# Kernel tuning notes

Hardware: AMD Instinct MI355X
Metric: run time of the kernel (lower is better)

## Reference

```python
import jax, jax.numpy as jnp
import numpy as np

B = 128          # graphs
N = 512          # nodes per graph
NT = B * N       # total nodes = 65536
E = NT * 16      # total edges = 1048576
IN = 64
H = 128
OUT = 2
L = 4            # num_layers
RATIO = 0.8


def setup_inputs() -> dict:
    key = jax.random.key(0)
    ks = jax.random.split(key, 20)

    def w(k, shape, fan_in):
        return jax.random.normal(k, shape, jnp.float32) / np.sqrt(fan_in)

    x = jax.random.normal(ks[0], (NT, IN), jnp.float32)
    edge_index = jax.random.randint(ks[1], (2, E), 0, NT, dtype=jnp.int32)
    batch = (jnp.arange(NT) // N).astype(jnp.int32)  # equal-size graphs

    return {
        "x": x,
        "edge_index": edge_index,
        "batch": batch,
        # conv1: GraphConv(IN, H, aggr='mean') -> lin_rel (w/ bias) + lin_root (no bias)
        "W1_rel": w(ks[2], (IN, H), IN),
        "W1_root": w(ks[3], (IN, H), IN),
        "b1": jnp.zeros((H,), jnp.float32),
        # convs[0..2]: GraphConv(H, H, aggr='mean'), stacked
        "Wc_rel": w(ks[4], (L - 1, H, H), H),
        "Wc_root": w(ks[5], (L - 1, H, H), H),
        "bc": jnp.zeros((L - 1, H), jnp.float32),
        # SAGPooling score GNN: GraphConv(H, 1) with default aggr='add'
        "pw_rel": w(ks[6], (H,), H),
        "pw_root": w(ks[7], (H,), H),
        "pb": jnp.zeros((1,), jnp.float32),
        # MLP head
        "lin1_W": w(ks[8], (L * H, H), L * H),
        "lin1_b": jnp.zeros((H,), jnp.float32),
        "lin2_W": w(ks[9], (H, OUT), H),
        "lin2_b": jnp.zeros((OUT,), jnp.float32),
    }


def _graph_conv_mean(x, src, dst, emask, W_rel, W_root, b, n):
    # PyG GraphConv: lin_rel(mean_{j->i} x_j) + lin_root(x_i); masked edges excluded.
    msg = x[src] * emask[:, None]                                  # [E, D] gather
    s = jax.ops.segment_sum(msg, dst, num_segments=n)              # [n, D] scatter-add
    cnt = jax.ops.segment_sum(emask, dst, num_segments=n)          # [n]
    agg = s / jnp.maximum(cnt, 1.0)[:, None]                       # zero for isolated nodes
    return agg @ W_rel + x @ W_root + b


def reference(x, edge_index, batch, W1_rel, W1_root, b1, Wc_rel, Wc_root, bc,
              pw_rel, pw_root, pb, lin1_W, lin1_b, lin2_W, lin2_b):
    src = edge_index[0]
    dst = edge_index[1]
    emask = jnp.ones((E,), jnp.float32)
    n = NT
    npg = N  # nodes per graph (all graphs equal size)

    h = jax.nn.relu(_graph_conv_mean(x, src, dst, emask, W1_rel, W1_root, b1, n))
    xs = [h.reshape(B, npg, H).mean(axis=1)]  # global_mean_pool

    for i in range(L - 1):
        h = jax.nn.relu(_graph_conv_mean(h, src, dst, emask, Wc_rel[i], Wc_root[i], bc[i], n))
        xs.append(h.reshape(B, npg, H).mean(axis=1))
        if i % 2 == 0 and i < L - 2:
            # ---- SAGPooling: score via GraphConv(H,1) with add aggregation ----
            smsg = jax.ops.segment_sum(h[src] * emask[:, None], dst, num_segments=n)
            score = smsg @ pw_rel + h @ pw_root + pb[0]            # [n]
            k = int(np.ceil(RATIO * npg))
            topv, topi = jax.lax.top_k(score.reshape(B, npg), k)   # per-graph top-k
            perm = (jnp.arange(B)[:, None] * npg + topi).reshape(-1)  # global kept ids
            h = h[perm] * jnp.tanh(topv.reshape(-1))[:, None]
            # remap edges; edges touching dropped nodes get masked out
            node_map = jnp.full((n,), -1, jnp.int32).at[perm].set(
                jnp.arange(B * k, dtype=jnp.int32))
            ns, nd = node_map[src], node_map[dst]
            keep = ((ns >= 0) & (nd >= 0)).astype(jnp.float32)
            emask = emask * keep
            src = jnp.where(ns >= 0, ns, 0)
            dst = jnp.where(nd >= 0, nd, 0)
            n = B * k
            npg = k

    xcat = jnp.concatenate(xs, axis=-1)                            # JumpingKnowledge 'cat'
    out = jax.nn.relu(xcat @ lin1_W + lin1_b)
    # dropout is identity in eval mode
    out = out @ lin2_W + lin2_b
    return jax.nn.log_softmax(out, axis=-1)
```

## Files before the change

### kernel.cpp

```cpp
#include <hip/hip_runtime.h>
#include <math.h>

#define NT 65536
#define EE 1048576
#define NB 128
#define KK 410
#define HH 128

typedef short bf16x8 __attribute__((ext_vector_type(8)));
typedef float f32x4 __attribute__((ext_vector_type(4)));

__device__ unsigned short g_xb[(size_t)NT * 64];
__device__ unsigned short g_hb1[(size_t)NT * HH];
__device__ unsigned short g_hb2[(size_t)NT * HH];
__device__ unsigned short g_wt1[128 * 128];
__device__ unsigned short g_wtc[3 * 128 * 256];
__device__ unsigned short g_csr1u[EE];
__device__ unsigned short g_keptu[NT];
__device__ unsigned int g_ebuck[EE];
__device__ int g_bcnt[128];
__device__ int g_bcur[128];
__device__ float g_trel[NT];
__device__ float g_troot[NT];
__device__ float g_gatef[NT];
__device__ float g_kinv[NT];
__device__ float g_xc16[4 * NB * 16 * 128];
__device__ int g_rows1[NT + 1];

__device__ __forceinline__ float b2f(unsigned short u) {
    union { unsigned int i; float f; } v;
    v.i = ((unsigned int)u) << 16;
    return v.f;
}
__device__ __forceinline__ unsigned short f2b(float f) {
    unsigned int x = __float_as_uint(f);
    unsigned int r = x + 0x7fffu + ((x >> 16) & 1u);
    return (unsigned short)(r >> 16);
}
__device__ __forceinline__ bf16x8 scale8(bf16x8 a, float g) {
    bf16x8 r;
#pragma unroll
    for (int i = 0; i < 8; i++) {
        unsigned short u = (unsigned short)a[i];
        r[i] = (short)f2b(b2f(u) * g);
    }
    return r;
}

__global__ __launch_bounds__(256) void k_prep(const float* __restrict__ x,
                                              const float* __restrict__ W1r,
                                              const float* __restrict__ W1o,
                                              const float* __restrict__ Wcr,
                                              const float* __restrict__ Wco,
                                              const int* __restrict__ dst) {
    if (blockIdx.x < 4544) {
        int tid = blockIdx.x * 256 + threadIdx.x;
        if (tid < 1048576) {
            float4 v = *(const float4*)&x[(size_t)tid * 4];
            unsigned int lo = (unsigned int)f2b(v.x) | ((unsigned int)f2b(v.y) << 16);
            unsigned int hi = (unsigned int)f2b(v.z) | ((unsigned int)f2b(v.w) << 16);
            *(uint2*)&g_xb[(size_t)tid * 4] = make_uint2(lo, hi);
        } else if (tid < 1048576 + 16384) {
            int r = tid - 1048576;
            int k = r & 127, n = r >> 7;
            float v = (k < 64) ? W1r[k * 128 + n] : W1o[(k - 64) * 128 + n];
            g_wt1[n * 128 + k] = f2b(v);
        } else {
            int r = tid - (1048576 + 16384);
            int l = r >> 15;
            int k = r & 255, n = (r >> 8) & 127;
            float v = (k < 128) ? Wcr[l * 16384 + k * 128 + n]
                                : Wco[l * 16384 + (k - 128) * 128 + n];
            g_wtc[l * 32768 + n * 256 + k] = f2b(v);
        }
    } else {
        __shared__ int h[128];
        if (threadIdx.x < 128) h[threadIdx.x] = 0;
        __syncthreads();
        int e0 = ((blockIdx.x - 4544) * 256 + threadIdx.x) * 4;
        int4 d = *(const int4*)&dst[e0];
        atomicAdd(&h[d.x >> 9], 1);
        atomicAdd(&h[d.y >> 9], 1);
        atomicAdd(&h[d.z >> 9], 1);
        atomicAdd(&h[d.w >> 9], 1);
        __syncthreads();
        if (threadIdx.x < 128 && h[threadIdx.x]) atomicAdd(&g_bcnt[threadIdx.x], h[threadIdx.x]);
    }
}

__global__ __launch_bounds__(256) void k_bscatter(const int* __restrict__ src,
                                                  const int* __restrict__ dst) {
    __shared__ int h[128];
    __shared__ int base[128];
    __shared__ int sc[128];
    __shared__ int vv[128];
    int t = threadIdx.x;
    if (t < 128) { vv[t] = g_bcnt[t]; sc[t] = vv[t]; h[t] = 0; }
    __syncthreads();
    for (int off = 1; off < 128; off <<= 1) {
        int u = (t >= off && t < 128) ? sc[t - off] : 0;
        __syncthreads();
        if (t < 128) sc[t] += u;
        __syncthreads();
    }
    int e0 = (blockIdx.x * 256 + t) * 4;
    int4 s = *(const int4*)&src[e0];
    int4 d = *(const int4*)&dst[e0];
    int b0 = d.x >> 9, b1 = d.y >> 9, b2 = d.z >> 9, b3 = d.w >> 9;
    atomicAdd(&h[b0], 1);
    atomicAdd(&h[b1], 1);
    atomicAdd(&h[b2], 1);
    atomicAdd(&h[b3], 1);
    __syncthreads();
    if (t < 128) {
        int c = h[t];
        base[t] = (sc[t] - vv[t]) + (c ? atomicAdd(&g_bcur[t], c) : 0);
        h[t] = 0;
    }
    __syncthreads();
    int r0 = atomicAdd(&h[b0], 1);
    g_ebuck[base[b0] + r0] = ((unsigned int)(d.x & 511) << 16) | (unsigned int)s.x;
    int r1 = atomicAdd(&h[b1], 1);
    g_ebuck[base[b1] + r1] = ((unsigned int)(d.y & 511) << 16) | (unsigned int)s.y;
    int r2 = atomicAdd(&h[b2], 1);
    g_ebuck[base[b2] + r2] = ((unsigned int)(d.z & 511) << 16) | (unsigned int)s.z;
    int r3 = atomicAdd(&h[b3], 1);
    g_ebuck[base[b3] + r3] = ((unsigned int)(d.w & 511) << 16) | (unsigned int)s.w;
}

__global__ __launch_bounds__(512) void k_bcsr() {
    __shared__ int hist[512];
    __shared__ int offs[512];
    __shared__ int cur[512];
    __shared__ int sc[128];
    int g = blockIdx.x, t = threadIdx.x;
    if (t < 128) sc[t] = g_bcnt[t];
    hist[t] = 0;
    cur[t] = 0;
    __syncthreads();
    for (int off = 1; off < 128; off <<= 1) {
        int u = (t >= off && t < 128) ? sc[t - off] : 0;
        __syncthreads();
        if (t < 128) sc[t] += u;
        __syncthreads();
    }
    int b0 = sc[g] - g_bcnt[g];
    int b1 = sc[g];
    for (int e = b0 + t; e < b1; e += 512) {
        unsigned int p = g_ebuck[e];
        atomicAdd(&hist[p >> 16], 1);
    }
    __syncthreads();
    int v = hist[t];
    offs[t] = v;
    __syncthreads();
    for (int off = 1; off < 512; off <<= 1) {
        int u = (t >= off) ? offs[t - off] : 0;
        __syncthreads();
        offs[t] += u;
        __syncthreads();
    }
    int excl = offs[t] - v;
    g_rows1[g * 512 + t] = b0 + excl;
    if (t == 511) g_rows1[g * 512 + 512] = b0 + excl + v;
    __syncthreads();
    offs[t] = excl;
    __syncthreads();
    for (int e = b0 + t; e < b1; e += 512) {
        unsigned int p = g_ebuck[e];
        int dl = p >> 16;
        int r = atomicAdd(&cur[dl], 1);
        g_csr1u[b0 + offs[dl] + r] = (unsigned short)(p & 0xFFFFu);
    }
}

__global__ __launch_bounds__(256, 4) void k_conv1(const float* __restrict__ bias) {
    const unsigned short* h = g_xb;
    const unsigned short* Wt = g_wt1;
    unsigned short* out = g_hb1;
    __shared__ float s[128];
    int lane = threadIdx.x & 63;
    int w = threadIdx.x >> 6;
    int n16 = lane & 15, quad = lane >> 4;
    int rowbase = blockIdx.x * 64;
    int rowg = rowbase + w * 16;
    int node = rowg + n16;
    if (threadIdx.x < 128) s[threadIdx.x] = 0.f;
    int r0 = g_rows1[node], r1 = g_rows1[node + 1];
    float aggacc[2][8];
#pragma unroll
    for (int ch = 0; ch < 2; ch++)
#pragma unroll
        for (int j = 0; j < 8; j++) aggacc[ch][j] = 0.f;
    const unsigned short* hq = h + quad * 8;
#define ACC8(arow, v)                                            \
    arow[0] += b2f((unsigned short)(v.x & 0xffff));              \
    arow[1] += b2f((unsigned short)(v.x >> 16));                 \
    arow[2] += b2f((unsigned short)(v.y & 0xffff));              \
    arow[3] += b2f((unsigned short)(v.y >> 16));                 \
    arow[4] += b2f((unsigned short)(v.z & 0xffff));              \
    arow[5] += b2f((unsigned short)(v.z >> 16));                 \
    arow[6] += b2f((unsigned short)(v.w & 0xffff));              \
    arow[7] += b2f((unsigned short)(v.w >> 16));
    int e = r0;
    for (; e + 2 <= r1; e += 2) {
        int i0 = g_csr1u[e], i1 = g_csr1u[e + 1];
        uint4 v00 = *(const uint4*)&hq[(size_t)i0 * 64];
        uint4 v01 = *(const uint4*)&hq[(size_t)i0 * 64 + 32];
        uint4 v10 = *(const uint4*)&hq[(size_t)i1 * 64];
        uint4 v11 = *(const uint4*)&hq[(size_t)i1 * 64 + 32];
        ACC8(aggacc[0], v00) ACC8(aggacc[1], v01)
        ACC8(aggacc[0], v10) ACC8(aggacc[1], v11)
    }
    if (e < r1) {
        int i0 = g_csr1u[e];
        uint4 v00 = *(const uint4*)&hq[(size_t)i0 * 64];
        uint4 v01 = *(const uint4*)&hq[(size_t)i0 * 64 + 32];
        ACC8(aggacc[0], v00) ACC8(aggacc[1], v01)
    }
#undef ACC8
    int c = r1 - r0;
    float inv = 1.0f / (float)(c > 0 ? c : 1);
    bf16x8 afrag[2];
#pragma unroll
    for (int ch = 0; ch < 2; ch++)
#pragma unroll
        for (int j = 0; j < 8; j++) afrag[ch][j] = (short)f2b(aggacc[ch][j] * inv);

    f32x4 acc[8];
#pragma unroll
    for (int ct = 0; ct < 8; ct++)
#pragma unroll
        for (int i = 0; i < 4; i++) acc[ct][i] = 0.f;
#pragma unroll
    for (int ks = 0; ks < 4; ks++) {
        bf16x8 a;
        if (ks < 2) a = afrag[ks];
        else a = *(const bf16x8*)&g_xb[(size_t)node * 64 + (ks - 2) * 32 + quad * 8];
#pragma unroll
        for (int ct = 0; ct < 8; ct++) {
            bf16x8 b = *(const bf16x8*)&Wt[(size_t)(ct * 16 + n16) * 128 + ks * 32 + quad * 8];
            acc[ct] = __builtin_amdgcn_mfma_f32_16x16x32_bf16(a, b, acc[ct], 0, 0, 0);
        }
    }
#pragma unroll
    for (int ct = 0; ct < 8; ct++) {
        int cc = ct * 16 + n16;
        float bv = bias[cc];
#pragma unroll
        for (int i = 0; i < 4; i++) {
            int r = rowg + quad * 4 + i;
            float v = fmaxf(acc[ct][i] + bv, 0.f);
            acc[ct][i] = v;
            out[(size_t)r * 128 + cc] = f2b(v);
        }
    }
    __syncthreads();
#pragma unroll
    for (int ct = 0; ct < 8; ct++) {
        float p = acc[ct][0] + acc[ct][1] + acc[ct][2] + acc[ct][3];
        p += __shfl_xor(p, 16);
        p += __shfl_xor(p, 32);
        if (quad == 0) atomicAdd(&s[ct * 16 + n16], p);
    }
    __syncthreads();
    if (threadIdx.x < 128) {
        int gr = blockIdx.x >> 3, e8 = blockIdx.x & 7;
        g_xc16[((0 * NB + gr) * 16 + e8) * 128 + threadIdx.x] = s[threadIdx.x];
    }
}

template <int KC, int GATED, int MASKED, int DOTS, int BGATE>
__global__ __launch_bounds__(256, 8) void k_conv(int hSel, int bSel, int wOfs,
                                                 const float* __restrict__ bias, int outSel,
                                                 int sec,
                                                 const float* __restrict__ pwr,
                                                 const float* __restrict__ pwt) {
    const unsigned short* h = hSel == 1 ? g_hb1 : g_hb2;
    const unsigned short* Bp = bSel == 1 ? g_hb1 : g_hb2;
    const unsigned short* Wt = g_wtc + wOfs;
    unsigned short* out = outSel == 1 ? g_hb1 : g_hb2;
    __shared__ unsigned short frag[2][16][136];
    __shared__ float s[128];
    __shared__ float sdr[32], sdt[32];
    int lane = threadIdx.x & 63;
    int w = threadIdx.x >> 6;
    int g = w >> 1;
    int h2 = w & 1;
    int n16 = lane & 15, quad = lane >> 4;
    int rowbase = blockIdx.x * 32;
    int rowg = rowbase + g * 16;
    int node = rowg + n16;
    if (threadIdx.x < 128) s[threadIdx.x] = 0.f;
    if (threadIdx.x < 32) { sdr[threadIdx.x] = 0.f; sdt[threadIdx.x] = 0.f; }

    int r0 = g_rows1[node], r1 = g_rows1[node + 1];
    float aggacc[2][8];
#pragma unroll
    for (int ch = 0; ch < 2; ch++)
#pragma unroll
        for (int j = 0; j < 8; j++) aggacc[ch][j] = 0.f;
    int kc = 0;
    const unsigned short* hq = h + h2 * 64 + quad * 8;
#define ACC8(arow, v, gf)                                        \
    arow[0] += gf * b2f((unsigned short)(v.x & 0xffff));         \
    arow[1] += gf * b2f((unsigned short)(v.x >> 16));            \
    arow[2] += gf * b2f((unsigned short)(v.y & 0xffff));         \
    arow[3] += gf * b2f((unsigned short)(v.y >> 16));            \
    arow[4] += gf * b2f((unsigned short)(v.z & 0xffff));         \
    arow[5] += gf * b2f((unsigned short)(v.z >> 16));            \
    arow[6] += gf * b2f((unsigned short)(v.w & 0xffff));         \
    arow[7] += gf * b2f((unsigned short)(v.w >> 16));
    int e = r0;
    for (; e + 2 <= r1; e += 2) {
        int i0 = g_csr1u[e], i1 = g_csr1u[e + 1];
        uint4 v00 = *(const uint4*)&hq[(size_t)i0 * 128];
        uint4 v01 = *(const uint4*)&hq[(size_t)i0 * 128 + 32];
        uint4 v10 = *(const uint4*)&hq[(size_t)i1 * 128];
        uint4 v11 = *(const uint4*)&hq[(size_t)i1 * 128 + 32];
        float gf0 = GATED ? g_gatef[i0] : 1.0f;
        float gf1 = GATED ? g_gatef[i1] : 1.0f;
        if (KC == 1) kc += (int)g_keptu[i0] + (int)g_keptu[i1];
        ACC8(aggacc[0], v00, gf0) ACC8(aggacc[1], v01, gf0)
        ACC8(aggacc[0], v10, gf1) ACC8(aggacc[1], v11, gf1)
    }
    if (e < r1) {
        int i0 = g_csr1u[e];
        uint4 v00 = *(const uint4*)&hq[(size_t)i0 * 128];
        uint4 v01 = *(const uint4*)&hq[(size_t)i0 * 128 + 32];
        float gf0 = GATED ? g_gatef[i0] : 1.0f;
        if (KC == 1) kc += (int)g_keptu[i0];
        ACC8(aggacc[0], v00, gf0) ACC8(aggacc[1], v01, gf0)
    }
#undef ACC8
    float inv;
    if (KC == 0) {
        int c = r1 - r0;
        inv = 1.0f / (float)(c > 0 ? c : 1);
    } else if (KC == 1) {
        inv = 1.0f / (float)(kc > 0 ? kc : 1);
        if (h2 == 0 && quad == 0) g_kinv[node] = inv;
    } else {
        inv = g_kinv[node];
    }
#pragma unroll
    for (int ch = 0; ch < 2; ch++) {
        bf16x8 fk;
#pragma unroll
        for (int j = 0; j < 8; j++) fk[j] = (short)f2b(aggacc[ch][j] * inv);
        *(bf16x8*)&frag[g][n16][h2 * 64 + ch * 32 + quad * 8] = fk;
    }
    __syncthreads();

    float ga = BGATE ? g_gatef[node] : 1.0f;
    f32x4 acc[4];
#pragma unroll
    for (int c4 = 0; c4 < 4; c4++)
#pragma unroll
        for (int i = 0; i < 4; i++) acc[c4][i] = 0.f;
#pragma unroll
    for (int ks = 0; ks < 8; ks++) {
        bf16x8 a;
        if (ks < 4) {
            a = *(const bf16x8*)&frag[g][n16][ks * 32 + quad * 8];
        } else {
            a = *(const bf16x8*)&Bp[(size_t)node * 128 + (ks - 4) * 32 + quad * 8];
            if (BGATE) a = scale8(a, ga);
        }
#pragma unroll
        for (int c4 = 0; c4 < 4; c4++) {
            int ct = h2 * 4 + c4;
            bf16x8 b = *(const bf16x8*)&Wt[(size_t)(ct * 16 + n16) * 256 + ks * 32 + quad * 8];
            acc[c4] = __builtin_amdgcn_mfma_f32_16x16x32_bf16(a, b, acc[c4], 0, 0, 0);
        }
    }

    {
        float m[4];
#pragma unroll
        for (int i = 0; i < 4; i++) {
            int r = rowg + quad * 4 + i;
            m[i] = (!MASKED || g_keptu[r]) ? 1.0f : 0.0f;
        }
#pragma unroll
        for (int c4 = 0; c4 < 4; c4++) {
            int c = (h2 * 4 + c4) * 16 + n16;
            float bv = bias[c];
#pragma unroll
            for (int i = 0; i < 4; i++) {
                int r = rowg + quad * 4 + i;
                float v = fmaxf(acc[c4][i] + bv, 0.f) * m[i];
                acc[c4][i] = v;
                out[(size_t)r * 128 + c] = f2b(v);
            }
        }
    }

#pragma unroll
    for (int c4 = 0; c4 < 4; c4++) {
        float p = acc[c4][0] + acc[c4][1] + acc[c4][2] + acc[c4][3];
        p += __shfl_xor(p, 16);
        p += __shfl_xor(p, 32);
        if (quad == 0) atomicAdd(&s[(h2 * 4 + c4) * 16 + n16], p);
    }

    if (DOTS) {
        float pr[4], pt[4];
#pragma unroll
        for (int c4 = 0; c4 < 4; c4++) {
            pr[c4] = pwr[(h2 * 4 + c4) * 16 + n16];
            pt[c4] = pwt[(h2 * 4 + c4) * 16 + n16];
        }
#pragma unroll
        for (int i = 0; i < 4; i++) {
            float dr = 0.f, dt = 0.f;
#pragma unroll
            for (int c4 = 0; c4 < 4; c4++) {
                dr += acc[c4][i] * pr[c4];
                dt += acc[c4][i] * pt[c4];
            }
            dr += __shfl_xor(dr, 1); dt += __shfl_xor(dt, 1);
            dr += __shfl_xor(dr, 2); dt += __shfl_xor(dt, 2);
            dr += __shfl_xor(dr, 4); dt += __shfl_xor(dt, 4);
            dr += __shfl_xor(dr, 8); dt += __shfl_xor(dt, 8);
            if (n16 == 0) {
                atomicAdd(&sdr[g * 16 + quad * 4 + i], dr);
                atomicAdd(&sdt[g * 16 + quad * 4 + i], dt);
            }
        }
    }
    __syncthreads();
    if (threadIdx.x < 128) {
        int gr = blockIdx.x >> 4, e16 = blockIdx.x & 15;
        g_xc16[((sec * NB + gr) * 16 + e16) * 128 + threadIdx.x] = s[threadIdx.x];
    }
    if (DOTS && threadIdx.x < 32) {
        g_trel[rowbase + threadIdx.x] = sdr[threadIdx.x];
        g_troot[rowbase + threadIdx.x] = sdt[threadIdx.x];
    }
}

__global__ __launch_bounds__(256) void k_topk(const float* __restrict__ pb) {
    __shared__ float sv[512];
    __shared__ int si[512];
    int g = blockIdx.x, t = threadIdx.x;
    if (t == 0) { g_bcnt[g] = 0; g_bcur[g] = 0; }
    float pbv = pb[0];
    for (int l = t; l < 512; l += 256) {
        int node = g * 512 + l;
        int r0 = g_rows1[node], r1 = g_rows1[node + 1];
        float s = 0.f;
        int e = r0;
        for (; e + 4 <= r1; e += 4) {
            float s0 = g_trel[g_csr1u[e]];
            float s1 = g_trel[g_csr1u[e + 1]];
            float s2 = g_trel[g_csr1u[e + 2]];
            float s3 = g_trel[g_csr1u[e + 3]];
            s += (s0 + s1) + (s2 + s3);
        }
        for (; e < r1; e++) s += g_trel[g_csr1u[e]];
        sv[l] = s + g_troot[node] + pbv;
        si[l] = l;
    }
    __syncthreads();
    for (int k = 2; k <= 512; k <<= 1) {
        for (int j = k >> 1; j > 0; j >>= 1) {
            for (int i = t; i < 512; i += 256) {
                int p = i ^ j;
                if (p > i) {
                    float va = sv[i], vb = sv[p];
                    int ia = si[i], ib = si[p];
                    bool aFirst = (va > vb) || (va == vb && ia < ib);
                    bool up = ((i & k) == 0);
                    if (up != aFirst) { sv[i] = vb; sv[p] = va; si[i] = ib; si[p] = ia; }
                }
            }
            __syncthreads();
        }
    }
    for (int r = t; r < 512; r += 256) {
        int old = g * 512 + si[r];
        if (r < KK) {
            g_gatef[old] = tanhf(sv[r]);
            g_keptu[old] = 1;
        } else {
            g_gatef[old] = 0.f;
            g_keptu[old] = 0;
        }
    }
}

__global__ __launch_bounds__(128) void k_head(const float* __restrict__ W1, const float* __restrict__ b1,
                                              const float* __restrict__ W2, const float* __restrict__ b2,
                                              float* __restrict__ out) {
    __shared__ float xr[512];
    __shared__ float r0[128], r1[128];
    int g = blockIdx.x, t = threadIdx.x;
    for (int i = t; i < 512; i += 128) {
        int sec = i >> 7, c = i & 127;
        const float* p = &g_xc16[((sec * NB + g) * 16) * 128 + c];
        int nq = (sec == 0) ? 8 : 16;
        float v = 0.f;
        for (int q = 0; q < nq; q++) v += p[q * 128];
        float inv = (sec < 2) ? (1.0f / 512.0f) : (1.0f / 410.0f);
        xr[i] = v * inv;
    }
    __syncthreads();
    float acc = b1[t];
    for (int k = 0; k < 512; k++) acc += xr[k] * W1[k * 128 + t];
    acc = fmaxf(acc, 0.f);
    r0[t] = acc * W2[t * 2 + 0];
    r1[t] = acc * W2[t * 2 + 1];
    __syncthreads();
    for (int off = 64; off > 0; off >>= 1) {
        if (t < off) { r0[t] += r0[t + off]; r1[t] += r1[t + off]; }
        __syncthreads();
    }
    if (t == 0) {
        float z0 = r0[0] + b2[0], z1 = r1[0] + b2[1];
        float m = fmaxf(z0, z1);
        float l = m + logf(expf(z0 - m) + expf(z1 - m));
        out[g * 2 + 0] = z0 - l;
        out[g * 2 + 1] = z1 - l;
    }
}

extern "C" void kernel_launch(void* const* d_in, const int* in_sizes, int n_in,
                              void* d_out, int out_size, void* d_ws, size_t ws_size,
                              hipStream_t stream) {
    const float* x = (const float*)d_in[0];
    const int* ei = (const int*)d_in[1];
    const int* src = ei;
    const int* dst = ei + EE;
    const float* W1r = (const float*)d_in[3];
    const float* W1o = (const float*)d_in[4];
    const float* b1 = (const float*)d_in[5];
    const float* Wcr = (const float*)d_in[6];
    const float* Wco = (const float*)d_in[7];
    const float* bc = (const float*)d_in[8];
    const float* pwr = (const float*)d_in[9];
    const float* pwt = (const float*)d_in[10];
    const float* pb = (const float*)d_in[11];
    const float* l1W = (const float*)d_in[12];
    const float* l1b = (const float*)d_in[13];
    const float* l2W = (const float*)d_in[14];
    const float* l2b = (const float*)d_in[15];
    float* out = (float*)d_out;

    k_prep<<<5568, 256, 0, stream>>>(x, W1r, W1o, Wcr, Wco, dst);

    k_bscatter<<<1024, 256, 0, stream>>>(src, dst);
    k_bcsr<<<128, 512, 0, stream>>>();

    k_conv1<<<1024, 256, 0, stream>>>(b1);

    k_conv<0, 0, 0, 1, 0><<<2048, 256, 0, stream>>>(1, 1, 0, bc, 2, 1, pwr, pwt);

    k_topk<<<NB, 256, 0, stream>>>(pb);

    k_conv<1, 1, 1, 0, 1><<<2048, 256, 0, stream>>>(2, 2, 32768, bc + 128, 1, 2, pwr, pwt);

    k_conv<2, 0, 1, 0, 0><<<2048, 256, 0, stream>>>(1, 1, 65536, bc + 256, 2, 3, pwr, pwt);

    k_head<<<NB, 128, 0, stream>>>(l1W, l1b, l2W, l2b, out);
}
```

Before: 527.2 us.

## Use 16-row conv blocks with full-row gathers and sort CSR neighbors by source

Each k_conv block now handles 16 rows instead of 32. Every wavefront aggregates 4 destination rows, with each lane gathering one 16-byte chunk of a full 128-wide row, so a neighbor row is read as one contiguous 256-byte access. The MFMA stage splits output columns across the 4 waves, and the grid doubles to 4096 blocks with 32 partial-sum slots per graph. The CSR build also sub-sorts each row's edges by the high bits of the source index, which should improve cache locality of the gathers. The cost is more blocks, more redundant weight loads per row, and a larger shared histogram in k_bcsr.

```diff
diff --git a/kernel.cpp b/kernel.cpp
--- a/kernel.cpp
+++ b/kernel.cpp
@@ -24,7 +24,7 @@
 __device__ float g_troot[NT];
 __device__ float g_gatef[NT];
 __device__ float g_kinv[NT];
-__device__ float g_xc16[4 * NB * 16 * 128];
+__device__ float g_xc32[4 * NB * 32 * 128];
 __device__ int g_rows1[NT + 1];
 
 __device__ __forceinline__ float b2f(unsigned short u) {
@@ -129,14 +129,13 @@
 }
 
 __global__ __launch_bounds__(512) void k_bcsr() {
-    __shared__ int hist[512];
-    __shared__ int offs[512];
-    __shared__ int cur[512];
+    __shared__ int hist[4096];
+    __shared__ int cur[4096];
     __shared__ int sc[128];
+    __shared__ int temp[512];
     int g = blockIdx.x, t = threadIdx.x;
     if (t < 128) sc[t] = g_bcnt[t];
-    hist[t] = 0;
-    cur[t] = 0;
+    for (int i = t; i < 4096; i += 512) { hist[i] = 0; cur[i] = 0; }
     __syncthreads();
     for (int off = 1; off < 128; off <<= 1) {
         int u = (t >= off && t < 128) ? sc[t - off] : 0;
@@ -146,31 +145,38 @@
     }
     int b0 = sc[g] - g_bcnt[g];
     int b1 = sc[g];
+    __syncthreads();
     for (int e = b0 + t; e < b1; e += 512) {
         unsigned int p = g_ebuck[e];
-        atomicAdd(&hist[p >> 16], 1);
-    }
-    __syncthreads();
-    int v = hist[t];
-    offs[t] = v;
+        int key = (int)((p >> 16) << 3) | (int)((p & 0xFFFFu) >> 13);
+        atomicAdd(&hist[key], 1);
+    }
+    __syncthreads();
+    int vals[8];
+    int s8 = 0;
+#pragma unroll
+    for (int j = 0; j < 8; j++) { vals[j] = hist[t * 8 + j]; s8 += vals[j]; }
+    temp[t] = s8;
     __syncthreads();
     for (int off = 1; off < 512; off <<= 1) {
-        int u = (t >= off) ? offs[t - off] : 0;
-        __syncthreads();
-        offs[t] += u;
-        __syncthreads();
-    }
-    int excl = offs[t] - v;
+        int u = (t >= off) ? temp[t - off] : 0;
+        __syncthreads();
+        temp[t] += u;
+        __syncthreads();
+    }
+    int excl = temp[t] - s8;
+    int run = excl;
+#pragma unroll
+    for (int j = 0; j < 8; j++) { int v = vals[j]; hist[t * 8 + j] = run; run += v; }
     g_rows1[g * 512 + t] = b0 + excl;
-    if (t == 511) g_rows1[g * 512 + 512] = b0 + excl + v;
-    __syncthreads();
-    offs[t] = excl;
+    if (t == 511) g_rows1[g * 512 + 512] = b0 + excl + s8;
     __syncthreads();
     for (int e = b0 + t; e < b1; e += 512) {
         unsigned int p = g_ebuck[e];
-        int dl = p >> 16;
-        int r = atomicAdd(&cur[dl], 1);
-        g_csr1u[b0 + offs[dl] + r] = (unsigned short)(p & 0xFFFFu);
+        unsigned int srcv = p & 0xFFFFu;
+        int key = (int)((p >> 16) << 3) | (int)(srcv >> 13);
+        int r = atomicAdd(&cur[key], 1);
+        g_csr1u[b0 + hist[key] + r] = (unsigned short)srcv;
     }
 }
 
@@ -266,7 +272,7 @@
     __syncthreads();
     if (threadIdx.x < 128) {
         int gr = blockIdx.x >> 3, e8 = blockIdx.x & 7;
-        g_xc16[((0 * NB + gr) * 16 + e8) * 128 + threadIdx.x] = s[threadIdx.x];
+        g_xc32[((0 * NB + gr) * 32 + e8) * 128 + threadIdx.x] = s[threadIdx.x];
     }
 }
 
@@ -280,98 +286,100 @@
     const unsigned short* Bp = bSel == 1 ? g_hb1 : g_hb2;
     const unsigned short* Wt = g_wtc + wOfs;
     unsigned short* out = outSel == 1 ? g_hb1 : g_hb2;
-    __shared__ unsigned short frag[2][16][136];
+    __shared__ unsigned short frag[16][136];
     __shared__ float s[128];
-    __shared__ float sdr[32], sdt[32];
+    __shared__ float sdr[16], sdt[16];
     int lane = threadIdx.x & 63;
     int w = threadIdx.x >> 6;
-    int g = w >> 1;
-    int h2 = w & 1;
+    int rowbase = blockIdx.x * 16;
+    if (threadIdx.x < 128) s[threadIdx.x] = 0.f;
+    if (threadIdx.x < 16) { sdr[threadIdx.x] = 0.f; sdt[threadIdx.x] = 0.f; }
+
+    {
+        int rl = lane >> 4;
+        int c16 = lane & 15;
+        int m = w * 4 + rl;
+        int row = rowbase + m;
+        int r0 = g_rows1[row], r1 = g_rows1[row + 1];
+        float kinv_pre = (KC == 2) ? g_kinv[row] : 0.f;
+        float acc8[8];
+#pragma unroll
+        for (int j = 0; j < 8; j++) acc8[j] = 0.f;
+        int kc = 0;
+        const unsigned short* hq = h + c16 * 8;
+#define ACC8(v, gf)                                              \
+    acc8[0] += gf * b2f((unsigned short)(v.x & 0xffff));         \
+    acc8[1] += gf * b2f((unsigned short)(v.x >> 16));            \
+    acc8[2] += gf * b2f((unsigned short)(v.y & 0xffff));         \
+    acc8[3] += gf * b2f((unsigned short)(v.y >> 16));            \
+    acc8[4] += gf * b2f((unsigned short)(v.z & 0xffff));         \
+    acc8[5] += gf * b2f((unsigned short)(v.z >> 16));            \
+    acc8[6] += gf * b2f((unsigned short)(v.w & 0xffff));         \
+    acc8[7] += gf * b2f((unsigned short)(v.w >> 16));
+        int e = r0;
+        for (; e + 4 <= r1; e += 4) {
+            int i0 = g_csr1u[e], i1 = g_csr1u[e + 1];
+            int i2 = g_csr1u[e + 2], i3 = g_csr1u[e + 3];
+            uint4 v0 = *(const uint4*)&hq[(size_t)i0 * 128];
+            uint4 v1 = *(const uint4*)&hq[(size_t)i1 * 128];
+            uint4 v2 = *(const uint4*)&hq[(size_t)i2 * 128];
+            uint4 v3 = *(const uint4*)&hq[(size_t)i3 * 128];
+            float g0 = GATED ? g_gatef[i0] : 1.0f;
+            float g1 = GATED ? g_gatef[i1] : 1.0f;
+            float g2 = GATED ? g_gatef[i2] : 1.0f;
+            float g3 = GATED ? g_gatef[i3] : 1.0f;
+            if (KC == 1)
+                kc += (int)g_keptu[i0] + (int)g_keptu[i1]
+                    + (int)g_keptu[i2] + (int)g_keptu[i3];
+            ACC8(v0, g0) ACC8(v1, g1) ACC8(v2, g2) ACC8(v3, g3)
+        }
+        for (; e < r1; e++) {
+            int i0 = g_csr1u[e];
+            uint4 v0 = *(const uint4*)&hq[(size_t)i0 * 128];
+            float g0 = GATED ? g_gatef[i0] : 1.0f;
+            if (KC == 1) kc += (int)g_keptu[i0];
+            ACC8(v0, g0)
+        }
+#undef ACC8
+        float inv;
+        if (KC == 0) {
+            int c = r1 - r0;
+            inv = 1.0f / (float)(c > 0 ? c : 1);
+        } else if (KC == 1) {
+            inv = 1.0f / (float)(kc > 0 ? kc : 1);
+            if (c16 == 0) g_kinv[row] = inv;
+        } else {
+            inv = kinv_pre;
+        }
+        bf16x8 fk;
+#pragma unroll
+        for (int j = 0; j < 8; j++) fk[j] = (short)f2b(acc8[j] * inv);
+        *(bf16x8*)&frag[m][c16 * 8] = fk;
+    }
+    __syncthreads();
+
     int n16 = lane & 15, quad = lane >> 4;
-    int rowbase = blockIdx.x * 32;
-    int rowg = rowbase + g * 16;
-    int node = rowg + n16;
-    if (threadIdx.x < 128) s[threadIdx.x] = 0.f;
-    if (threadIdx.x < 32) { sdr[threadIdx.x] = 0.f; sdt[threadIdx.x] = 0.f; }
-
-    int r0 = g_rows1[node], r1 = g_rows1[node + 1];
-    float aggacc[2][8];
-#pragma unroll
-    for (int ch = 0; ch < 2; ch++)
-#pragma unroll
-        for (int j = 0; j < 8; j++) aggacc[ch][j] = 0.f;
-    int kc = 0;
-    const unsigned short* hq = h + h2 * 64 + quad * 8;
-#define ACC8(arow, v, gf)                                        \
-    arow[0] += gf * b2f((unsigned short)(v.x & 0xffff));         \
-    arow[1] += gf * b2f((unsigned short)(v.x >> 16));            \
-    arow[2] += gf * b2f((unsigned short)(v.y & 0xffff));         \
-    arow[3] += gf * b2f((unsigned short)(v.y >> 16));            \
-    arow[4] += gf * b2f((unsigned short)(v.z & 0xffff));         \
-    arow[5] += gf * b2f((unsigned short)(v.z >> 16));            \
-    arow[6] += gf * b2f((unsigned short)(v.w & 0xffff));         \
-    arow[7] += gf * b2f((unsigned short)(v.w >> 16));
-    int e = r0;
-    for (; e + 2 <= r1; e += 2) {
-        int i0 = g_csr1u[e], i1 = g_csr1u[e + 1];
-        uint4 v00 = *(const uint4*)&hq[(size_t)i0 * 128];
-        uint4 v01 = *(const uint4*)&hq[(size_t)i0 * 128 + 32];
-        uint4 v10 = *(const uint4*)&hq[(size_t)i1 * 128];
-        uint4 v11 = *(const uint4*)&hq[(size_t)i1 * 128 + 32];
-        float gf0 = GATED ? g_gatef[i0] : 1.0f;
-        float gf1 = GATED ? g_gatef[i1] : 1.0f;
-        if (KC == 1) kc += (int)g_keptu[i0] + (int)g_keptu[i1];
-        ACC8(aggacc[0], v00, gf0) ACC8(aggacc[1], v01, gf0)
-        ACC8(aggacc[0], v10, gf1) ACC8(aggacc[1], v11, gf1)
-    }
-    if (e < r1) {
-        int i0 = g_csr1u[e];
-        uint4 v00 = *(const uint4*)&hq[(size_t)i0 * 128];
-        uint4 v01 = *(const uint4*)&hq[(size_t)i0 * 128 + 32];
-        float gf0 = GATED ? g_gatef[i0] : 1.0f;
-        if (KC == 1) kc += (int)g_keptu[i0];
-        ACC8(aggacc[0], v00, gf0) ACC8(aggacc[1], v01, gf0)
-    }
-#undef ACC8
-    float inv;
-    if (KC == 0) {
-        int c = r1 - r0;
-        inv = 1.0f / (float)(c > 0 ? c : 1);
-    } else if (KC == 1) {
-        inv = 1.0f / (float)(kc > 0 ? kc : 1);
-        if (h2 == 0 && quad == 0) g_kinv[node] = inv;
-    } else {
-        inv = g_kinv[node];
-    }
-#pragma unroll
-    for (int ch = 0; ch < 2; ch++) {
-        bf16x8 fk;
-#pragma unroll
-        for (int j = 0; j < 8; j++) fk[j] = (short)f2b(aggacc[ch][j] * inv);
-        *(bf16x8*)&frag[g][n16][h2 * 64 + ch * 32 + quad * 8] = fk;
-    }
-    __syncthreads();
-
+    int node = rowbase + n16;
     float ga = BGATE ? g_gatef[node] : 1.0f;
-    f32x4 acc[4];
-#pragma unroll
-    for (int c4 = 0; c4 < 4; c4++)
-#pragma unroll
-        for (int i = 0; i < 4; i++) acc[c4][i] = 0.f;
+    f32x4 acc[2];
+#pragma unroll
+    for (int c2 = 0; c2 < 2; c2++)
+#pragma unroll
+        for (int i = 0; i < 4; i++) acc[c2][i] = 0.f;
 #pragma unroll
     for (int ks = 0; ks < 8; ks++) {
         bf16x8 a;
         if (ks < 4) {
-            a = *(const bf16x8*)&frag[g][n16][ks * 32 + quad * 8];
+            a = *(const bf16x8*)&frag[n16][ks * 32 + quad * 8];
         } else {
             a = *(const bf16x8*)&Bp[(size_t)node * 128 + (ks - 4) * 32 + quad * 8];
             if (BGATE) a = scale8(a, ga);
         }
 #pragma unroll
-        for (int c4 = 0; c4 < 4; c4++) {
-            int ct = h2 * 4 + c4;
+        for (int c2 = 0; c2 < 2; c2++) {
+            int ct = w * 2 + c2;
             bf16x8 b = *(const bf16x8*)&Wt[(size_t)(ct * 16 + n16) * 256 + ks * 32 + quad * 8];
-            acc[c4] = __builtin_amdgcn_mfma_f32_16x16x32_bf16(a, b, acc[c4], 0, 0, 0);
+            acc[c2] = __builtin_amdgcn_mfma_f32_16x16x32_bf16(a, b, acc[c2], 0, 0, 0);
         }
     }
 
@@ -379,62 +387,58 @@
         float m[4];
 #pragma unroll
         for (int i = 0; i < 4; i++) {
-            int r = rowg + quad * 4 + i;
+            int r = rowbase + quad * 4 + i;
             m[i] = (!MASKED || g_keptu[r]) ? 1.0f : 0.0f;
         }
 #pragma unroll
-        for (int c4 = 0; c4 < 4; c4++) {
-            int c = (h2 * 4 + c4) * 16 + n16;
+        for (int c2 = 0; c2 < 2; c2++) {
+            int c = (w * 2 + c2) * 16 + n16;
             float bv = bias[c];
 #pragma unroll
             for (int i = 0; i < 4; i++) {
-                int r = rowg + quad * 4 + i;
-                float v = fmaxf(acc[c4][i] + bv, 0.f) * m[i];
-                acc[c4][i] = v;
+                int r = rowbase + quad * 4 + i;
+                float v = fmaxf(acc[c2][i] + bv, 0.f) * m[i];
+                acc[c2][i] = v;
                 out[(size_t)r * 128 + c] = f2b(v);
             }
         }
     }
 
 #pragma unroll
-    for (int c4 = 0; c4 < 4; c4++) {
-        float p = acc[c4][0] + acc[c4][1] + acc[c4][2] + acc[c4][3];
+    for (int c2 = 0; c2 < 2; c2++) {
+        float p = acc[c2][0] + acc[c2][1] + acc[c2][2] + acc[c2][3];
         p += __shfl_xor(p, 16);
         p += __shfl_xor(p, 32);
-        if (quad == 0) atomicAdd(&s[(h2 * 4 + c4) * 16 + n16], p);
+        if (quad == 0) atomicAdd(&s[(w * 2 + c2) * 16 + n16], p);
     }
 
     if (DOTS) {
-        float pr[4], pt[4];
-#pragma unroll
-        for (int c4 = 0; c4 < 4; c4++) {
-            pr[c4] = pwr[(h2 * 4 + c4) * 16 + n16];
-            pt[c4] = pwt[(h2 * 4 + c4) * 16 + n16];
+        float pr[2], pt[2];
+#pragma unroll
+        for (int c2 = 0; c2 < 2; c2++) {
+            pr[c2] = pwr[(w * 2 + c2) * 16 + n16];
+            pt[c2] = pwt[(w * 2 + c2) * 16 + n16];
         }
 #pragma unroll
         for (int i = 0; i < 4; i++) {
-            float dr = 0.f, dt = 0.f;
-#pragma unroll
-            for (int c4 = 0; c4 < 4; c4++) {
-                dr += acc[c4][i] * pr[c4];
-                dt += acc[c4][i] * pt[c4];
-            }
+            float dr = acc[0][i] * pr[0] + acc[1][i] * pr[1];
+            float dt = acc[0][i] * pt[0] + acc[1][i] * pt[1];
             dr += __shfl_xor(dr, 1); dt += __shfl_xor(dt, 1);
             dr += __shfl_xor(dr, 2); dt += __shfl_xor(dt, 2);
             dr += __shfl_xor(dr, 4); dt += __shfl_xor(dt, 4);
             dr += __shfl_xor(dr, 8); dt += __shfl_xor(dt, 8);
             if (n16 == 0) {
-                atomicAdd(&sdr[g * 16 + quad * 4 + i], dr);
-                atomicAdd(&sdt[g * 16 + quad * 4 + i], dt);
+                atomicAdd(&sdr[quad * 4 + i], dr);
+                atomicAdd(&sdt[quad * 4 + i], dt);
             }
         }
     }
     __syncthreads();
     if (threadIdx.x < 128) {
-        int gr = blockIdx.x >> 4, e16 = blockIdx.x & 15;
-        g_xc16[((sec * NB + gr) * 16 + e16) * 128 + threadIdx.x] = s[threadIdx.x];
-    }
-    if (DOTS && threadIdx.x < 32) {
+        int gr = blockIdx.x >> 5, slot = blockIdx.x & 31;
+        g_xc32[((sec * NB + gr) * 32 + slot) * 128 + threadIdx.x] = s[threadIdx.x];
+    }
+    if (DOTS && threadIdx.x < 16) {
         g_trel[rowbase + threadIdx.x] = sdr[threadIdx.x];
         g_troot[rowbase + threadIdx.x] = sdt[threadIdx.x];
     }
@@ -498,8 +502,8 @@
     int g = blockIdx.x, t = threadIdx.x;
     for (int i = t; i < 512; i += 128) {
         int sec = i >> 7, c = i & 127;
-        const float* p = &g_xc16[((sec * NB + g) * 16) * 128 + c];
-        int nq = (sec == 0) ? 8 : 16;
+        const float* p = &g_xc32[((sec * NB + g) * 32) * 128 + c];
+        int nq = (sec == 0) ? 8 : 32;
         float v = 0.f;
         for (int q = 0; q < nq; q++) v += p[q * 128];
         float inv = (sec < 2) ? (1.0f / 512.0f) : (1.0f / 410.0f);
@@ -554,13 +558,13 @@
 
     k_conv1<<<1024, 256, 0, stream>>>(b1);
 
-    k_conv<0, 0, 0, 1, 0><<<2048, 256, 0, stream>>>(1, 1, 0, bc, 2, 1, pwr, pwt);
+    k_conv<0, 0, 0, 1, 0><<<4096, 256, 0, stream>>>(1, 1, 0, bc, 2, 1, pwr, pwt);
 
     k_topk<<<NB, 256, 0, stream>>>(pb);
 
-    k_conv<1, 1, 1, 0, 1><<<2048, 256, 0, stream>>>(2, 2, 32768, bc + 128, 1, 2, pwr, pwt);
-
-    k_conv<2, 0, 1, 0, 0><<<2048, 256, 0, stream>>>(1, 1, 65536, bc + 256, 2, 3, pwr, pwt);
+    k_conv<1, 1, 1, 0, 1><<<4096, 256, 0, stream>>>(2, 2, 32768, bc + 128, 1, 2, pwr, pwt);
+
+    k_conv<2, 0, 1, 0, 0><<<4096, 256, 0, stream>>>(1, 1, 65536, bc + 256, 2, 3, pwr, pwt);
 
     k_head<<<NB, 128, 0, stream>>>(l1W, l1b, l2W, l2b, out);
 }
```

Result: faster. 511.1 us (-3.1%).
